# Optimization experiments

Measured on AMD Instinct MI355X. Metric: run time of the kernel, lower is better.

Reference implementation:

```python
import jax, jax.numpy as jnp
import numpy as np

ALPHA, BETA, THETA = 1.0, 1.0, 10.0
WIN_SIZE = 11
SIGMA = 1.5


def _gauss_window(size, sigma, channel):
    g = np.exp(-((np.arange(size) - size // 2) ** 2) / (2.0 * sigma ** 2))
    g = g / g.sum()
    w2 = np.outer(g, g).astype(np.float32)  # [k, k]
    return jnp.asarray(np.tile(w2[None, None], (channel, 1, 1, 1)))  # [C,1,k,k]


def _dwconv_valid(x, w):
    # x: [B,C,H,W], w: [C,1,k,k]; depthwise conv, no padding (matches F.conv2d padd=0, groups=C)
    return jax.lax.conv_general_dilated(
        x, w, window_strides=(1, 1), padding='VALID',
        feature_group_count=x.shape[1],
        dimension_numbers=('NCHW', 'OIHW', 'NCHW'))


def _ssim_loss(img1, img2, window):
    # val_range heuristic: inputs in [0,1) -> L = 1
    L = 1.0
    C1 = (0.01 * L) ** 2
    C2 = (0.03 * L) ** 2
    mu1 = _dwconv_valid(img1, window)
    mu2 = _dwconv_valid(img2, window)
    mu1_sq = mu1 * mu1
    mu2_sq = mu2 * mu2
    mu1_mu2 = mu1 * mu2
    sigma1_sq = _dwconv_valid(img1 * img1, window) - mu1_sq
    sigma2_sq = _dwconv_valid(img2 * img2, window) - mu2_sq
    sigma12 = _dwconv_valid(img1 * img2, window) - mu1_mu2
    v1 = 2.0 * sigma12 + C2
    v2 = sigma1_sq + sigma2_sq + C2
    ssim_map = (2.0 * mu1_mu2 + C1) * v1 / ((mu1_sq + mu2_sq + C1) * v2)
    return 1.0 - jnp.mean(ssim_map)


_LAP2D = np.array([[1.0, 1.0, 1.0],
                   [1.0, -8.0, 1.0],
                   [1.0, 1.0, 1.0]], dtype=np.float32) / 16.0  # kornia normalized (abs-sum=16)


def _laplacian(x):
    # kornia.filters.laplacian(x, 3): reflect padding, normalized 3x3 laplacian, depthwise
    c = x.shape[1]
    k = jnp.asarray(np.tile(_LAP2D[None, None], (c, 1, 1, 1)))  # [C,1,3,3]
    xp = jnp.pad(x, ((0, 0), (0, 0), (1, 1), (1, 1)), mode='reflect')
    return _dwconv_valid(xp, k)


def setup_inputs() -> dict:
    key = jax.random.key(0)
    ks = jax.random.split(key, 5)
    shape = (32, 1, 512, 512)
    names = ['im_fus', 'im_ir', 'im_vi', 'map_ir', 'map_vi']
    return {n: jax.random.uniform(k, shape, dtype=jnp.float32) for n, k in zip(names, ks)}


def reference(im_fus, im_ir, im_vi, map_ir, map_vi):
    window = _gauss_window(WIN_SIZE, SIGMA, im_fus.shape[1])
    ms_ssim_loss = _ssim_loss(im_fus, im_ir, window) + _ssim_loss(im_fus, im_vi, window)
    l1_loss = jnp.mean(jnp.abs(jnp.maximum(map_ir, map_vi) - im_fus))
    ir_grad = jnp.abs(_laplacian(im_ir))
    vi_grad = jnp.abs(_laplacian(im_vi))
    fus_grad = jnp.abs(_laplacian(im_fus))
    grad_loss = jnp.mean(jnp.abs(jnp.maximum(ir_grad, vi_grad) - fus_grad))
    return ALPHA * ms_ssim_loss + BETA * l1_loss + THETA * grad_loss
```

## Files before the change

kernel.cpp:

```cpp
#include <hip/hip_runtime.h>
#include <cmath>


typedef float f32x2 __attribute__((ext_vector_type(2)));

struct GaussW { float w[11]; };

#define SSIM_C1 1.0e-4f
#define SSIM_C2 9.0e-4f

__global__ __launch_bounds__(256, 2)
void ssim_kernel(const float* __restrict__ fus, const float* __restrict__ irp,
                 const float* __restrict__ vip, const float* __restrict__ mir,
                 const float* __restrict__ mvi, float* __restrict__ ws,
                 GaussW gw)
{
    const int b    = blockIdx.z;
    const int rs   = blockIdx.y;
    const int r0   = rs * 42;
    const int tid  = threadIdx.x;
    const int wv   = tid >> 6;
    const int lane = tid & 63;
    const int c0   = blockIdx.x * 256 + wv * 64;
    const int out_rows = min(42, 502 - r0);
    const int in_rows  = out_rows + 10;
    const bool first = (rs == 0);
    const bool last  = (rs == 11);

    const size_t ib = (size_t)b * 512 * 512;
    const float* __restrict__ Fp = fus + ib;
    const float* __restrict__ Ip = irp + ib;
    const float* __restrict__ Vp = vip + ib;
    mir += ib;
    mvi += ib;

    __shared__ f32x2 srow_fi[4][2][80];
    __shared__ float srow_v [4][2][80];

    float w6[6];
#pragma unroll
    for (int k = 0; k < 6; ++k) w6[k] = gw.w[k];

    f32x2 acc[11][4];
#pragma unroll
    for (int s = 0; s < 11; ++s)
#pragma unroll
        for (int q = 0; q < 4; ++q) acc[s][q] = (f32x2)(0.f);

    float lssim = 0.f, l1s = 0.f, grs = 0.f;
    const int  col      = c0 + lane;
    const bool col_ok   = col <= 501;
    const bool is_left  = (lane == 10);
    const int  colH     = is_left ? (c0 - 1) : (c0 + 64 + lane);
    const bool halo_ok  = (lane < 10) ? (colH < 512) : (is_left && c0 > 0);
    const int  hidx     = 64 + lane;
    const int il       = (lane == 0) ? ((c0 == 0) ? 1 : 74) : (lane - 1);
    const bool rt_edge = (lane == 63) && (c0 + 64 >= 512);

    f32x2 csFI_1 = (f32x2)(0.f), csFI_2 = (f32x2)(0.f);
    float csV_1 = 0.f, csV_2 = 0.f;
    f32x2 cPrevFI = (f32x2)(0.f); float cPrevV = 0.f;
    float mA1 = 0.f, mA2 = 0.f, mB1, mB2;

    float arf, arg, arv, arf2 = 0.f, arg2 = 0.f, arv2 = 0.f;
    float brf, brg, brv, brf2 = 0.f, brg2 = 0.f, brv2 = 0.f;
    {
        const size_t b0 = (size_t)r0 * 512 + col;
        arf = Fp[b0]; arg = Ip[b0]; arv = Vp[b0];
        const size_t b1 = (size_t)(r0 + 1) * 512 + col;
        brf = Fp[b1]; brg = Ip[b1]; brv = Vp[b1];
        if (halo_ok) {
            const size_t h0 = (size_t)r0 * 512 + colH;
            arf2 = Fp[h0]; arg2 = Ip[h0]; arv2 = Vp[h0];
            const size_t h1 = (size_t)(r0 + 1) * 512 + colH;
            brf2 = Fp[h1]; brg2 = Ip[h1]; brv2 = Vp[h1];
        }
        mB1 = mir[b0]; mB2 = mvi[b0];
    }

#pragma unroll 1
    for (int rb = 0; rb < 66; rb += 22) {
#pragma unroll
        for (int p = 0; p < 11; ++p) {
            const int r = rb + 2 * p;
            if (r < in_rows) {
                srow_fi[wv][0][lane] = (f32x2){arf, arg};
                srow_v [wv][0][lane] = arv;
                srow_fi[wv][1][lane] = (f32x2){brf, brg};
                srow_v [wv][1][lane] = brv;
                if (halo_ok) {
                    srow_fi[wv][0][hidx] = (f32x2){arf2, arg2};
                    srow_v [wv][0][hidx] = arv2;
                    srow_fi[wv][1][hidx] = (f32x2){brf2, brg2};
                    srow_v [wv][1][hidx] = brv2;
                }
                __builtin_amdgcn_wave_barrier();

                if (r + 2 < in_rows) {
                    const size_t bA = (size_t)(r0 + r + 2) * 512 + col;
                    arf = Fp[bA]; arg = Ip[bA]; arv = Vp[bA];
                    const size_t bB = (size_t)(r0 + r + 3) * 512 + col;
                    brf = Fp[bB]; brg = Ip[bB]; brv = Vp[bB];
                    if (halo_ok) {
                        const size_t hA = (size_t)(r0 + r + 2) * 512 + colH;
                        arf2 = Fp[hA]; arg2 = Ip[hA]; arv2 = Vp[hA];
                        const size_t hB = (size_t)(r0 + r + 3) * 512 + colH;
                        brf2 = Fp[hB]; brg2 = Ip[hB]; brv2 = Vp[hB];
                    }
                }

                f32x2 hfhiA = (f32x2)(0.f), hffiiA = (f32x2)(0.f);
                f32x2 hfifvA = (f32x2)(0.f), hvvvA = (f32x2)(0.f);
                f32x2 hfhiB = (f32x2)(0.f), hffiiB = (f32x2)(0.f);
                f32x2 hfifvB = (f32x2)(0.f), hvvvB = (f32x2)(0.f);
                f32x2 fi0A = (f32x2)(0.f), fi1A = (f32x2)(0.f);
                f32x2 fi0B = (f32x2)(0.f), fi1B = (f32x2)(0.f);
                float v0A = 0.f, v1A = 0.f, v0B = 0.f, v1B = 0.f;
#pragma unroll
                for (int k = 0; k < 11; ++k) {
                    const float t = w6[k < 6 ? k : 10 - k];
                    const f32x2 t2 = (f32x2){t, t};
                    const f32x2 fiA = srow_fi[wv][0][lane + k];
                    const float VA  = srow_v [wv][0][lane + k];
                    const f32x2 fiB = srow_fi[wv][1][lane + k];
                    const float VB  = srow_v [wv][1][lane + k];
                    if (k == 0) { fi0A = fiA; v0A = VA; fi0B = fiB; v0B = VB; }
                    if (k == 1) { fi1A = fiA; v1A = VA; fi1B = fiB; v1B = VB; }
                    const f32x2 tfiA = t2 * fiA;
                    hfhiA  = __builtin_elementwise_fma(t2,   fiA, hfhiA);
                    hffiiA = __builtin_elementwise_fma(tfiA, fiA, hffiiA);
                    hfifvA.x = fmaf(tfiA.x, fiA.y, hfifvA.x);
                    hfifvA.y = fmaf(tfiA.x, VA,    hfifvA.y);
                    hvvvA.x = fmaf(t,      VA, hvvvA.x);
                    hvvvA.y = fmaf(t * VA, VA, hvvvA.y);
                    const f32x2 tfiB = t2 * fiB;
                    hfhiB  = __builtin_elementwise_fma(t2,   fiB, hfhiB);
                    hffiiB = __builtin_elementwise_fma(tfiB, fiB, hffiiB);
                    hfifvB.x = fmaf(tfiB.x, fiB.y, hfifvB.x);
                    hfifvB.y = fmaf(tfiB.x, VB,    hfifvB.y);
                    hvvvB.x = fmaf(t,      VB, hvvvB.x);
                    hvvvB.y = fmaf(t * VB, VB, hvvvB.y);
                }

                const bool lap = (r <= 43) || last;
                f32x2 csA_FI = (f32x2)(0.f), csB_FI = (f32x2)(0.f);
                float csA_V = 0.f, csB_V = 0.f;
                if (lap) {
                    const f32x2 fiLA = srow_fi[wv][0][il];
                    const float vLA  = srow_v [wv][0][il];
                    const f32x2 fiLB = srow_fi[wv][1][il];
                    const float vLB  = srow_v [wv][1][il];
                    f32x2 fiRA = fi1A; float vRA = v1A;
                    f32x2 fiRB = fi1B; float vRB = v1B;
                    if (rt_edge) { fiRA = fiLA; vRA = vLA; fiRB = fiLB; vRB = vLB; }
                    csA_FI = fiLA + fiRA + fi0A;  csA_V = vLA + vRA + v0A;
                    csB_FI = fiLB + fiRB + fi0B;  csB_V = vLB + vRB + v0B;
                }
                __builtin_amdgcn_wave_barrier();

                {
                    const f32x2 w02 = (f32x2){w6[0], w6[0]};
                    acc[(2*p) % 11][0] = w02 * hfhiA;
                    acc[(2*p) % 11][1] = w02 * hffiiA;
                    acc[(2*p) % 11][2] = w02 * hfifvA;
                    acc[(2*p) % 11][3] = w02 * hvvvA;
                }
#pragma unroll
                for (int k = 1; k < 11; ++k) {
                    const int s = (2*p - k + 22) % 11;
                    const float t = w6[k < 6 ? k : 10 - k];
                    const f32x2 t2 = (f32x2){t, t};
                    acc[s][0] = __builtin_elementwise_fma(t2, hfhiA,  acc[s][0]);
                    acc[s][1] = __builtin_elementwise_fma(t2, hffiiA, acc[s][1]);
                    acc[s][2] = __builtin_elementwise_fma(t2, hfifvA, acc[s][2]);
                    acc[s][3] = __builtin_elementwise_fma(t2, hvvvA,  acc[s][3]);
                }
                if (r >= 10) {
                    const int s = (2*p + 1) % 11;
                    const float mu1 = acc[s][0].x, mu2 = acc[s][0].y, mu3 = acc[s][3].x;
                    const float eff = acc[s][1].x, eii = acc[s][1].y, evv = acc[s][3].y;
                    const float efi = acc[s][2].x, efv = acc[s][2].y;
                    const float mu1sq = mu1*mu1, mu2sq = mu2*mu2, mu3sq = mu3*mu3;
                    const float mu12 = mu1*mu2, mu13 = mu1*mu3;
                    const float sf  = eff - mu1sq;
                    const float si  = eii - mu2sq;
                    const float sv  = evv - mu3sq;
                    const float s12 = efi - mu12;
                    const float s13 = efv - mu13;
                    const float n1 = (2.f*mu12 + SSIM_C1) * (2.f*s12 + SSIM_C2);
                    const float d1 = (mu1sq + mu2sq + SSIM_C1) * (sf + si + SSIM_C2);
                    const float n2 = (2.f*mu13 + SSIM_C1) * (2.f*s13 + SSIM_C2);
                    const float d2 = (mu1sq + mu3sq + SSIM_C1) * (sf + sv + SSIM_C2);
                    const float q1 = __builtin_amdgcn_rcpf(d1);
                    const float q2 = __builtin_amdgcn_rcpf(d2);
                    if (col_ok) lssim += fmaf(n1, q1, n2 * q2);
                }
                {
                    const f32x2 w02 = (f32x2){w6[0], w6[0]};
                    acc[(2*p + 1) % 11][0] = w02 * hfhiB;
                    acc[(2*p + 1) % 11][1] = w02 * hffiiB;
                    acc[(2*p + 1) % 11][2] = w02 * hfifvB;
                    acc[(2*p + 1) % 11][3] = w02 * hvvvB;
                }
#pragma unroll
                for (int k = 1; k < 11; ++k) {
                    const int s = (2*p + 1 - k + 22) % 11;
                    const float t = w6[k < 6 ? k : 10 - k];
                    const f32x2 t2 = (f32x2){t, t};
                    acc[s][0] = __builtin_elementwise_fma(t2, hfhiB,  acc[s][0]);
                    acc[s][1] = __builtin_elementwise_fma(t2, hffiiB, acc[s][1]);
                    acc[s][2] = __builtin_elementwise_fma(t2, hfifvB, acc[s][2]);
                    acc[s][3] = __builtin_elementwise_fma(t2, hvvvB,  acc[s][3]);
                }
                if (r >= 10) {
                    const int s = (2*p + 2) % 11;
                    const float mu1 = acc[s][0].x, mu2 = acc[s][0].y, mu3 = acc[s][3].x;
                    const float eff = acc[s][1].x, eii = acc[s][1].y, evv = acc[s][3].y;
                    const float efi = acc[s][2].x, efv = acc[s][2].y;
                    const float mu1sq = mu1*mu1, mu2sq = mu2*mu2, mu3sq = mu3*mu3;
                    const float mu12 = mu1*mu2, mu13 = mu1*mu3;
                    const float sf  = eff - mu1sq;
                    const float si  = eii - mu2sq;
                    const float sv  = evv - mu3sq;
                    const float s12 = efi - mu12;
                    const float s13 = efv - mu13;
                    const float n1 = (2.f*mu12 + SSIM_C1) * (2.f*s12 + SSIM_C2);
                    const float d1 = (mu1sq + mu2sq + SSIM_C1) * (sf + si + SSIM_C2);
                    const float n2 = (2.f*mu13 + SSIM_C1) * (2.f*s13 + SSIM_C2);
                    const float d2 = (mu1sq + mu3sq + SSIM_C1) * (sf + sv + SSIM_C2);
                    const float q1 = __builtin_amdgcn_rcpf(d1);
                    const float q2 = __builtin_amdgcn_rcpf(d2);
                    if (col_ok) lssim += fmaf(n1, q1, n2 * q2);
                }

                if (lap) {
                    if (r >= 2) {
                        const f32x2 sFI = csFI_2 + csFI_1 + csA_FI;
                        const float sV  = csV_2 + csV_1 + csA_V;
                        const f32x2 lFI = __builtin_elementwise_fma(
                                             (f32x2){-9.f,-9.f}, cPrevFI, sFI);
                        const float lV  = fmaf(-9.f, cPrevV, sV);
                        grs += fabsf(fmaxf(fabsf(lFI.y), fabsf(lV)) - fabsf(lFI.x));
                        l1s += fabsf(fmaxf(mA1, mA2) - cPrevFI.x);
                        const f32x2 sFI2 = csFI_1 + csA_FI + csB_FI;
                        const float sV2  = csV_1 + csA_V + csB_V;
                        const f32x2 lFI2 = __builtin_elementwise_fma(
                                             (f32x2){-9.f,-9.f}, fi0A, sFI2);
                        const float lV2  = fmaf(-9.f, v0A, sV2);
                        grs += fabsf(fmaxf(fabsf(lFI2.y), fabsf(lV2)) - fabsf(lFI2.x));
                        l1s += fabsf(fmaxf(mB1, mB2) - fi0A.x);
                    }
                    if (first && r == 0) {
                        const f32x2 sFI = csA_FI + csB_FI + csB_FI;
                        const float sV  = csA_V + csB_V + csB_V;
                        const f32x2 lFI = __builtin_elementwise_fma(
                                             (f32x2){-9.f,-9.f}, fi0A, sFI);
                        const float lV  = fmaf(-9.f, v0A, sV);
                        grs += fabsf(fmaxf(fabsf(lFI.y), fabsf(lV)) - fabsf(lFI.x));
                        l1s += fabsf(fmaxf(mB1, mB2) - fi0A.x);
                    }
                    csFI_2 = csA_FI; csFI_1 = csB_FI;
                    csV_2  = csA_V;  csV_1  = csB_V;
                    cPrevFI = fi0B;  cPrevV = v0B;
                    if (r + 2 < in_rows) {
                        const int yA = min(r0 + r + 1, 511);
                        const int yB = min(r0 + r + 2, 511);
                        const size_t bmA = (size_t)yA * 512 + col;
                        const size_t bmB = (size_t)yB * 512 + col;
                        mA1 = mir[bmA]; mA2 = mvi[bmA];
                        mB1 = mir[bmB]; mB2 = mvi[bmB];
                    }
                }
            }
        }
    }

    if (last) {
        const size_t bm = (size_t)511 * 512 + col;
        const float m1e = mir[bm], m2e = mvi[bm];
        const f32x2 sFI = csFI_2 + csFI_2 + csFI_1;
        const float sV  = csV_2 + csV_2 + csV_1;
        const f32x2 lFI = __builtin_elementwise_fma((f32x2){-9.f,-9.f}, cPrevFI, sFI);
        const float lV  = fmaf(-9.f, cPrevV, sV);
        grs += fabsf(fmaxf(fabsf(lFI.y), fabsf(lV)) - fabsf(lFI.x));
        l1s += fabsf(fmaxf(m1e, m2e) - cPrevFI.x);
    }

#pragma unroll
    for (int off = 32; off > 0; off >>= 1) {
        lssim += __shfl_down(lssim, off);
        l1s   += __shfl_down(l1s, off);
        grs   += __shfl_down(grs, off);
    }
    __shared__ float red[12];
    if (lane == 0) { red[wv] = lssim; red[4 + wv] = l1s; red[8 + wv] = grs; }
    __syncthreads();
    if (tid == 0) {
        const int blk = blockIdx.x + 2 * (blockIdx.y + 12 * blockIdx.z);
        ws[blk]        = red[0] + red[1] + red[2] + red[3];
        ws[768 + blk]  = red[4] + red[5] + red[6] + red[7];
        ws[1536 + blk] = (red[8] + red[9] + red[10] + red[11]) * 0.0625f;
    }
}

__global__ void final_kernel(const float* __restrict__ ws, float* __restrict__ out)
{
    const int tid = threadIdx.x;
    float s0 = 0.f, s1 = 0.f, s2 = 0.f;
#pragma unroll
    for (int i = tid; i < 768; i += 256) {
        s0 += ws[i];
        s1 += ws[768 + i];
        s2 += ws[1536 + i];
    }
#pragma unroll
    for (int off = 32; off > 0; off >>= 1) {
        s0 += __shfl_down(s0, off);
        s1 += __shfl_down(s1, off);
        s2 += __shfl_down(s2, off);
    }
    __shared__ float red[12];
    if ((tid & 63) == 0) {
        red[tid >> 6] = s0; red[4 + (tid >> 6)] = s1; red[8 + (tid >> 6)] = s2;
    }
    __syncthreads();
    if (tid == 0) {
        const float ssim_sum = red[0] + red[1] + red[2] + red[3];
        const float l1_sum   = red[4] + red[5] + red[6] + red[7];
        const float gr_sum   = red[8] + red[9] + red[10] + red[11];
        const float ms = 2.f - ssim_sum / 8064128.f;
        const float l1 = l1_sum / 8388608.f;
        const float gr = gr_sum / 8388608.f;
        out[0] = ms + l1 + 10.f * gr;
    }
}

extern "C" void kernel_launch(void* const* d_in, const int* in_sizes, int n_in,
                              void* d_out, int out_size, void* d_ws, size_t ws_size,
                              hipStream_t stream)
{
    const float* fus = (const float*)d_in[0];
    const float* irp = (const float*)d_in[1];
    const float* vip = (const float*)d_in[2];
    const float* mir = (const float*)d_in[3];
    const float* mvi = (const float*)d_in[4];
    float* out = (float*)d_out;
    float* ws  = (float*)d_ws;

    GaussW gw;
    double g[11], s = 0.0;
    for (int i = 0; i < 11; ++i) {
        const double d = (double)i - 5.0;
        g[i] = std::exp(-(d * d) / (2.0 * 1.5 * 1.5));
        s += g[i];
    }
    for (int i = 0; i < 11; ++i) gw.w[i] = (float)(g[i] / s);

    ssim_kernel<<<dim3(2, 12, 32), 256, 0, stream>>>(fus, irp, vip, mir, mvi,
                                                     ws, gw);
    final_kernel<<<1, 256, 0, stream>>>(ws, out);
}
```

Measured before the change: 89.97 us.

## Double-buffer per-wave LDS row staging and prefetch rows two steps ahead

Per-wave shared-memory row buffers gain a second slot. The next row pair is written into the alternate slot after the current horizontal pass, and global loads for rows r+4/r+5 are issued early, so load latency overlaps more compute. This removes the store-then-read dependency at the top of each iteration at the cost of double the LDS footprint and longer register live ranges for the prefetched values.

```diff
diff --git a/kernel.cpp b/kernel.cpp
--- a/kernel.cpp
+++ b/kernel.cpp
@@ -34,8 +34,8 @@
     mir += ib;
     mvi += ib;
 
-    __shared__ f32x2 srow_fi[4][2][80];
-    __shared__ float srow_v [4][2][80];
+    __shared__ f32x2 srow_fi[4][2][2][80];
+    __shared__ float srow_v [4][2][2][80];
 
     float w6[6];
 #pragma unroll
@@ -76,7 +76,29 @@
             brf2 = Fp[h1]; brg2 = Ip[h1]; brv2 = Vp[h1];
         }
         mB1 = mir[b0]; mB2 = mvi[b0];
-    }
+        srow_fi[wv][0][0][lane] = (f32x2){arf, arg};
+        srow_v [wv][0][0][lane] = arv;
+        srow_fi[wv][0][1][lane] = (f32x2){brf, brg};
+        srow_v [wv][0][1][lane] = brv;
+        if (halo_ok) {
+            srow_fi[wv][0][0][hidx] = (f32x2){arf2, arg2};
+            srow_v [wv][0][0][hidx] = arv2;
+            srow_fi[wv][0][1][hidx] = (f32x2){brf2, brg2};
+            srow_v [wv][0][1][hidx] = brv2;
+        }
+        const size_t b2 = (size_t)(r0 + 2) * 512 + col;
+        arf = Fp[b2]; arg = Ip[b2]; arv = Vp[b2];
+        const size_t b3 = (size_t)(r0 + 3) * 512 + col;
+        brf = Fp[b3]; brg = Ip[b3]; brv = Vp[b3];
+        if (halo_ok) {
+            const size_t h2 = (size_t)(r0 + 2) * 512 + colH;
+            arf2 = Fp[h2]; arg2 = Ip[h2]; arv2 = Vp[h2];
+            const size_t h3 = (size_t)(r0 + 3) * 512 + colH;
+            brf2 = Fp[h3]; brg2 = Ip[h3]; brv2 = Vp[h3];
+        }
+    }
+    __builtin_amdgcn_wave_barrier();
+    int cur = 0;
 
 #pragma unroll 1
     for (int rb = 0; rb < 66; rb += 22) {
@@ -84,31 +106,6 @@
         for (int p = 0; p < 11; ++p) {
             const int r = rb + 2 * p;
             if (r < in_rows) {
-                srow_fi[wv][0][lane] = (f32x2){arf, arg};
-                srow_v [wv][0][lane] = arv;
-                srow_fi[wv][1][lane] = (f32x2){brf, brg};
-                srow_v [wv][1][lane] = brv;
-                if (halo_ok) {
-                    srow_fi[wv][0][hidx] = (f32x2){arf2, arg2};
-                    srow_v [wv][0][hidx] = arv2;
-                    srow_fi[wv][1][hidx] = (f32x2){brf2, brg2};
-                    srow_v [wv][1][hidx] = brv2;
-                }
-                __builtin_amdgcn_wave_barrier();
-
-                if (r + 2 < in_rows) {
-                    const size_t bA = (size_t)(r0 + r + 2) * 512 + col;
-                    arf = Fp[bA]; arg = Ip[bA]; arv = Vp[bA];
-                    const size_t bB = (size_t)(r0 + r + 3) * 512 + col;
-                    brf = Fp[bB]; brg = Ip[bB]; brv = Vp[bB];
-                    if (halo_ok) {
-                        const size_t hA = (size_t)(r0 + r + 2) * 512 + colH;
-                        arf2 = Fp[hA]; arg2 = Ip[hA]; arv2 = Vp[hA];
-                        const size_t hB = (size_t)(r0 + r + 3) * 512 + colH;
-                        brf2 = Fp[hB]; brg2 = Ip[hB]; brv2 = Vp[hB];
-                    }
-                }
-
                 f32x2 hfhiA = (f32x2)(0.f), hffiiA = (f32x2)(0.f);
                 f32x2 hfifvA = (f32x2)(0.f), hvvvA = (f32x2)(0.f);
                 f32x2 hfhiB = (f32x2)(0.f), hffiiB = (f32x2)(0.f);
@@ -120,10 +117,10 @@
                 for (int k = 0; k < 11; ++k) {
                     const float t = w6[k < 6 ? k : 10 - k];
                     const f32x2 t2 = (f32x2){t, t};
-                    const f32x2 fiA = srow_fi[wv][0][lane + k];
-                    const float VA  = srow_v [wv][0][lane + k];
-                    const f32x2 fiB = srow_fi[wv][1][lane + k];
-                    const float VB  = srow_v [wv][1][lane + k];
+                    const f32x2 fiA = srow_fi[wv][cur][0][lane + k];
+                    const float VA  = srow_v [wv][cur][0][lane + k];
+                    const f32x2 fiB = srow_fi[wv][cur][1][lane + k];
+                    const float VB  = srow_v [wv][cur][1][lane + k];
                     if (k == 0) { fi0A = fiA; v0A = VA; fi0B = fiB; v0B = VB; }
                     if (k == 1) { fi1A = fiA; v1A = VA; fi1B = fiB; v1B = VB; }
                     const f32x2 tfiA = t2 * fiA;
@@ -146,10 +143,10 @@
                 f32x2 csA_FI = (f32x2)(0.f), csB_FI = (f32x2)(0.f);
                 float csA_V = 0.f, csB_V = 0.f;
                 if (lap) {
-                    const f32x2 fiLA = srow_fi[wv][0][il];
-                    const float vLA  = srow_v [wv][0][il];
-                    const f32x2 fiLB = srow_fi[wv][1][il];
-                    const float vLB  = srow_v [wv][1][il];
+                    const f32x2 fiLA = srow_fi[wv][cur][0][il];
+                    const float vLA  = srow_v [wv][cur][0][il];
+                    const f32x2 fiLB = srow_fi[wv][cur][1][il];
+                    const float vLB  = srow_v [wv][cur][1][il];
                     f32x2 fiRA = fi1A; float vRA = v1A;
                     f32x2 fiRB = fi1B; float vRB = v1B;
                     if (rt_edge) { fiRA = fiLA; vRA = vLA; fiRB = fiLB; vRB = vLB; }
@@ -157,6 +154,33 @@
                     csB_FI = fiLB + fiRB + fi0B;  csB_V = vLB + vRB + v0B;
                 }
                 __builtin_amdgcn_wave_barrier();
+
+                if (r + 2 < in_rows) {
+                    srow_fi[wv][cur ^ 1][0][lane] = (f32x2){arf, arg};
+                    srow_v [wv][cur ^ 1][0][lane] = arv;
+                    srow_fi[wv][cur ^ 1][1][lane] = (f32x2){brf, brg};
+                    srow_v [wv][cur ^ 1][1][lane] = brv;
+                    if (halo_ok) {
+                        srow_fi[wv][cur ^ 1][0][hidx] = (f32x2){arf2, arg2};
+                        srow_v [wv][cur ^ 1][0][hidx] = arv2;
+                        srow_fi[wv][cur ^ 1][1][hidx] = (f32x2){brf2, brg2};
+                        srow_v [wv][cur ^ 1][1][hidx] = brv2;
+                    }
+                }
+                __builtin_amdgcn_wave_barrier();
+
+                if (r + 4 < in_rows) {
+                    const size_t bA = (size_t)(r0 + r + 4) * 512 + col;
+                    arf = Fp[bA]; arg = Ip[bA]; arv = Vp[bA];
+                    const size_t bB = (size_t)(r0 + r + 5) * 512 + col;
+                    brf = Fp[bB]; brg = Ip[bB]; brv = Vp[bB];
+                    if (halo_ok) {
+                        const size_t hA = (size_t)(r0 + r + 4) * 512 + colH;
+                        arf2 = Fp[hA]; arg2 = Ip[hA]; arv2 = Vp[hA];
+                        const size_t hB = (size_t)(r0 + r + 5) * 512 + colH;
+                        brf2 = Fp[hB]; brg2 = Ip[hB]; brv2 = Vp[hB];
+                    }
+                }
 
                 {
                     const f32x2 w02 = (f32x2){w6[0], w6[0]};
@@ -271,6 +295,7 @@
                         mB1 = mir[bmB]; mB2 = mvi[bmB];
                     }
                 }
+                cur ^= 1;
             }
         }
     }
```

New measurement: 91.66 us. Within noise of the previous version (+1.9%).
